# Kernel tuning notes

Measured on AMD Instinct MI355X. Metric: run time of the kernel, lower is better.

## Reference

```python
import jax, jax.numpy as jnp
import numpy as np
from jax import lax

B, S, H = 2, 1024, 1024
I = 512            # moe_intermediate_size
E = 32             # n_routed_experts
TOP_K = 4
N_GROUP = 4
TOPK_GROUP = 2
SCALE = 2.5        # routed_scaling_factor
N_SHARED = 2
SH_I = I * N_SHARED


def setup_inputs() -> dict:
    key = jax.random.key(0)
    ks = jax.random.split(key, 10)
    std = 0.02
    return {
        "hidden_states": jax.random.normal(ks[0], (B, S, H), jnp.float32),
        "router_weight": jax.random.normal(ks[1], (E, H), jnp.float32) * std,
        "router_bias": jnp.zeros((E,), jnp.float32),
        "gate_w": jax.random.normal(ks[2], (E, I, H), jnp.float32) * std,
        "up_w": jax.random.normal(ks[3], (E, I, H), jnp.float32) * std,
        "down_w": jax.random.normal(ks[4], (E, H, I), jnp.float32) * std,
        "shared_gate_w": jax.random.normal(ks[5], (SH_I, H), jnp.float32) * std,
        "shared_up_w": jax.random.normal(ks[6], (SH_I, H), jnp.float32) * std,
        "shared_down_w": jax.random.normal(ks[7], (H, SH_I), jnp.float32) * std,
    }


def _route(tokens, router_weight, router_bias):
    # tokens: [T, H] -> topk_idx [T, K] int, topk_weight [T, K] f32
    logits = tokens.astype(jnp.float32) @ router_weight.astype(jnp.float32).T  # [T, E]
    scores = jax.nn.sigmoid(logits)
    sfc = scores + router_bias[None, :]
    T = tokens.shape[0]
    # group scores: sum of top-2 per group
    grp = sfc.reshape(T, N_GROUP, E // N_GROUP)
    group_scores = lax.top_k(grp, 2)[0].sum(-1)                 # [T, n_group]
    _, gidx = lax.top_k(group_scores, TOPK_GROUP)               # [T, topk_group]
    gmask = jax.nn.one_hot(gidx, N_GROUP, dtype=sfc.dtype).sum(1)  # [T, n_group]
    smask = jnp.broadcast_to(gmask[:, :, None], (T, N_GROUP, E // N_GROUP)).reshape(T, E)
    tmp = jnp.where(smask > 0, sfc, 0.0)
    _, topk_idx = lax.top_k(tmp, TOP_K)                         # [T, K]
    topk_w = jnp.take_along_axis(scores, topk_idx, axis=1)
    topk_w = topk_w / (topk_w.sum(-1, keepdims=True) + 1e-20)   # norm_topk_prob
    topk_w = topk_w * SCALE
    return topk_idx, topk_w


def reference(hidden_states, router_weight, router_bias, gate_w, up_w, down_w,
              shared_gate_w, shared_up_w, shared_down_w):
    tokens = hidden_states.reshape(-1, H)                       # [T, H]
    topk_idx, topk_w = _route(tokens, router_weight, router_bias)
    # dense all-expert SwiGLU
    gate_vals = jax.nn.silu(jnp.einsum('th,eih->tei', tokens, gate_w))
    up_vals = jnp.einsum('th,eih->tei', tokens, up_w)
    hidden_vals = gate_vals * up_vals                           # [T, E, I]
    expert_out = jnp.einsum('tei,ehi->teh', hidden_vals, down_w)  # [T, E, H]
    sel = jnp.take_along_axis(expert_out, topk_idx[:, :, None], axis=1)  # [T, K, H]
    mixed = (sel * topk_w[:, :, None].astype(sel.dtype)).sum(1)
    mixed = mixed.reshape(hidden_states.shape)
    # shared experts (dense SwiGLU MLP)
    sg = jax.nn.silu(jnp.einsum('bsh,ih->bsi', hidden_states, shared_gate_w))
    su = jnp.einsum('bsh,ih->bsi', hidden_states, shared_up_w)
    shared = jnp.einsum('bsi,hi->bsh', sg * su, shared_down_w)
    return mixed + shared
```

## Files before the change

kernel.cpp:

```cpp
#include <hip/hip_runtime.h>
#include <hip/hip_bf16.h>
#include <math.h>

#define HD 1024
#define ID 512
#define NE 32
#define NT 2048
#define NG 4
#define SHI 1024
#define SCALE 2.5f

#define BN 64
#define BK 32
#define LDA 40

typedef __bf16 bf16_t;
typedef __attribute__((ext_vector_type(8))) __bf16 bf16x8;
typedef __attribute__((ext_vector_type(4))) __bf16 bf16x4;
typedef __attribute__((ext_vector_type(4))) float f32x4;

#define LTOK 8
#define LKC 64
__global__ void __launch_bounds__(256) logits_kernel(
    const float* __restrict__ hs, const float* __restrict__ rw,
    float* __restrict__ logits, int* __restrict__ counts)
{
    if (blockIdx.x == 0 && threadIdx.x < NE) counts[threadIdx.x] = 0;

    __shared__ float Xs[LTOK][68];
    __shared__ float Ws[NE][65];

    int tid = threadIdx.x;
    int t0 = blockIdx.x * LTOK;
    int tslot = tid >> 5, ecol = tid & 31;
    float acc = 0.f;

    for (int k0 = 0; k0 < HD; k0 += LKC) {
        if (tid < 128) {
            int row = tid >> 4, q = tid & 15;
            float4 v = *(const float4*)(hs + (size_t)(t0 + row) * HD + k0 + q * 4);
            *(float4*)(&Xs[row][q * 4]) = v;
        }
        #pragma unroll
        for (int i = 0; i < 8; ++i) {
            int idx = i * 256 + tid;
            int e = idx >> 6, kk = idx & 63;
            Ws[e][kk] = rw[(size_t)e * HD + k0 + kk];
        }
        __syncthreads();
        #pragma unroll 8
        for (int kk = 0; kk < LKC; ++kk)
            acc += Xs[tslot][kk] * Ws[ecol][kk];
        __syncthreads();
    }
    logits[(size_t)(t0 + tslot) * NE + ecol] = acc;
}

__global__ void __launch_bounds__(256) topk_kernel(
    const float* __restrict__ logits, const float* __restrict__ rb,
    float* __restrict__ topkw, int* __restrict__ counts, int* __restrict__ lists)
{
    int t = blockIdx.x * 256 + threadIdx.x;
    if (t >= NT) return;

    float scores[NE], sfc[NE], tmp[NE];
    #pragma unroll
    for (int e = 0; e < NE; ++e) {
        float l = logits[(size_t)t * NE + e];
        float s = 1.f / (1.f + __expf(-l));
        scores[e] = s;
        sfc[e] = s + rb[e];
    }
    float gs[NG];
    #pragma unroll
    for (int g = 0; g < NG; ++g) {
        float m1 = -1e30f, m2 = -1e30f;
        #pragma unroll
        for (int j = 0; j < 8; ++j) {
            float v = sfc[g * 8 + j];
            if (v > m1) { m2 = m1; m1 = v; } else if (v > m2) m2 = v;
        }
        gs[g] = m1 + m2;
    }
    int g1 = 0;
    #pragma unroll
    for (int g = 1; g < NG; ++g) if (gs[g] > gs[g1]) g1 = g;
    int g2 = -1;
    #pragma unroll
    for (int g = 0; g < NG; ++g) {
        if (g == g1) continue;
        if (g2 < 0 || gs[g] > gs[g2]) g2 = g;
    }
    #pragma unroll
    for (int e = 0; e < NE; ++e) {
        int g = e >> 3;
        tmp[e] = (g == g1 || g == g2) ? sfc[e] : 0.0f;
    }
    int idx[4]; float wk[4]; float wsum = 0.f;
    #pragma unroll
    for (int k = 0; k < 4; ++k) {
        int best = 0; float bv = -1e30f;
        #pragma unroll
        for (int e = 0; e < NE; ++e) if (tmp[e] > bv) { bv = tmp[e]; best = e; }
        idx[k] = best; tmp[best] = -1e30f;
        wk[k] = scores[best]; wsum += wk[k];
    }
    float inv = SCALE / (wsum + 1e-20f);
    #pragma unroll
    for (int k = 0; k < 4; ++k) {
        int p = t * 4 + k;
        topkw[p] = wk[k] * inv;
        int e = idx[k];
        int pos = atomicAdd(&counts[e], 1);
        lists[e * NT + pos] = p;
    }
}

__device__ inline bf16x4 cvt4(float4 v) {
    bf16x4 r;
    r[0] = (__bf16)v.x; r[1] = (__bf16)v.y; r[2] = (__bf16)v.z; r[3] = (__bf16)v.w;
    return r;
}

template<bool EXPERT, int ND, int BMT>
__global__ void __launch_bounds__(256) gateup_mfma(
    const float* __restrict__ X, const float* __restrict__ Wg,
    const float* __restrict__ Wu, bf16_t* __restrict__ Hout,
    const int* __restrict__ lists, const int* __restrict__ counts)
{
    int e = 0, cnt = NT;
    const float* wg = Wg; const float* wu = Wu;
    if (EXPERT) {
        e = blockIdx.x; cnt = counts[e];
        wg = Wg + (size_t)e * ND * HD;
        wu = Wu + (size_t)e * ND * HD;
    }
    int mtb = blockIdx.y, ntb = blockIdx.z;
    if (mtb * BMT >= cnt) return;

    __shared__ __align__(16) bf16_t As[BMT * LDA];
    __shared__ __align__(16) bf16_t Bgs[BN * LDA];
    __shared__ __align__(16) bf16_t Bus[BN * LDA];
    __shared__ int rowid[BMT];

    int tid = threadIdx.x;
    if (tid < BMT) {
        int gm = mtb * BMT + tid;
        int mm = gm < cnt ? gm : cnt - 1;
        rowid[tid] = EXPERT ? lists[e * NT + mm] : mm;
    }
    __syncthreads();

    constexpr int AR = (BMT * BK) / (256 * 4);
    constexpr int BR = (BN * BK) / (256 * 4);
    constexpr int MT = BMT / 32;

    int lane = tid & 63;
    int w = tid >> 6;
    int wm = w & 1, wn = w >> 1;
    int lrow = lane & 15, quad = lane >> 4;

    f32x4 accg[MT][2], accu[MT][2];
    #pragma unroll
    for (int i = 0; i < MT; ++i)
        #pragma unroll
        for (int j = 0; j < 2; ++j) { accg[i][j] = (f32x4){0,0,0,0}; accu[i][j] = (f32x4){0,0,0,0}; }

    float4 pa[AR], pbg[BR], pbu[BR];

    #pragma unroll
    for (int r = 0; r < AR; ++r) {
        int idx = r * 256 + tid;
        int row = idx >> 3, kq = idx & 7;
        int tok = EXPERT ? (rowid[row] >> 2) : rowid[row];
        pa[r] = *(const float4*)(X + (size_t)tok * HD + kq * 4);
    }
    #pragma unroll
    for (int r = 0; r < BR; ++r) {
        int idx = r * 256 + tid;
        int n = idx >> 3, kq = idx & 7;
        size_t off = (size_t)(ntb * BN + n) * HD + kq * 4;
        pbg[r] = *(const float4*)(wg + off);
        pbu[r] = *(const float4*)(wu + off);
    }

    for (int k0 = 0; k0 < HD; k0 += BK) {
        #pragma unroll
        for (int r = 0; r < AR; ++r) {
            int idx = r * 256 + tid;
            int row = idx >> 3, kq = idx & 7;
            *(bf16x4*)(As + row * LDA + kq * 4) = cvt4(pa[r]);
        }
        #pragma unroll
        for (int r = 0; r < BR; ++r) {
            int idx = r * 256 + tid;
            int n = idx >> 3, kq = idx & 7;
            *(bf16x4*)(Bgs + n * LDA + kq * 4) = cvt4(pbg[r]);
            *(bf16x4*)(Bus + n * LDA + kq * 4) = cvt4(pbu[r]);
        }
        __syncthreads();

        int k1 = k0 + BK;
        if (k1 < HD) {
            #pragma unroll
            for (int r = 0; r < AR; ++r) {
                int idx = r * 256 + tid;
                int row = idx >> 3, kq = idx & 7;
                int tok = EXPERT ? (rowid[row] >> 2) : rowid[row];
                pa[r] = *(const float4*)(X + (size_t)tok * HD + k1 + kq * 4);
            }
            #pragma unroll
            for (int r = 0; r < BR; ++r) {
                int idx = r * 256 + tid;
                int n = idx >> 3, kq = idx & 7;
                size_t off = (size_t)(ntb * BN + n) * HD + k1 + kq * 4;
                pbg[r] = *(const float4*)(wg + off);
                pbu[r] = *(const float4*)(wu + off);
            }
        }

        bf16x8 af[MT], bg[2], bu[2];
        #pragma unroll
        for (int mt = 0; mt < MT; ++mt)
            af[mt] = *(const bf16x8*)(As + (wm * (BMT / 2) + mt * 16 + lrow) * LDA + quad * 8);
        #pragma unroll
        for (int nt = 0; nt < 2; ++nt) {
            bg[nt] = *(const bf16x8*)(Bgs + (wn * 32 + nt * 16 + lrow) * LDA + quad * 8);
            bu[nt] = *(const bf16x8*)(Bus + (wn * 32 + nt * 16 + lrow) * LDA + quad * 8);
        }
        #pragma unroll
        for (int mt = 0; mt < MT; ++mt)
            #pragma unroll
            for (int nt = 0; nt < 2; ++nt) {
                accg[mt][nt] = __builtin_amdgcn_mfma_f32_16x16x32_bf16(af[mt], bg[nt], accg[mt][nt], 0, 0, 0);
                accu[mt][nt] = __builtin_amdgcn_mfma_f32_16x16x32_bf16(af[mt], bu[nt], accu[mt][nt], 0, 0, 0);
            }
        __syncthreads();
    }

    #pragma unroll
    for (int mt = 0; mt < MT; ++mt)
        #pragma unroll
        for (int r = 0; r < 4; ++r) {
            int row_local = wm * (BMT / 2) + mt * 16 + quad * 4 + r;
            int gm = mtb * BMT + row_local;
            if (gm >= cnt) continue;
            int p = rowid[row_local];
            #pragma unroll
            for (int nt = 0; nt < 2; ++nt) {
                int col = ntb * BN + wn * 32 + nt * 16 + lrow;
                float g = accg[mt][nt][r], u = accu[mt][nt][r];
                float h = (g / (1.f + __expf(-g))) * u;
                Hout[(size_t)p * ND + col] = (__bf16)h;
            }
        }
}

template<bool EXPERT, int KD, int BMT>
__global__ void __launch_bounds__(256) down_mfma(
    const bf16_t* __restrict__ Hin, const float* __restrict__ Wd,
    float* __restrict__ out, const int* __restrict__ lists,
    const int* __restrict__ counts, const float* __restrict__ topkw)
{
    int e = 0, cnt = NT;
    const float* wd = Wd;
    if (EXPERT) {
        e = blockIdx.x; cnt = counts[e];
        wd = Wd + (size_t)e * HD * KD;
    }
    int mtb = blockIdx.y, ntb = blockIdx.z;
    if (mtb * BMT >= cnt) return;

    __shared__ __align__(16) bf16_t As[BMT * LDA];
    __shared__ __align__(16) bf16_t Ws[BN * LDA];
    __shared__ int rowid[BMT];

    int tid = threadIdx.x;
    if (tid < BMT) {
        int gm = mtb * BMT + tid;
        int mm = gm < cnt ? gm : cnt - 1;
        rowid[tid] = EXPERT ? lists[e * NT + mm] : mm;
    }
    __syncthreads();

    constexpr int ARH = (BMT * BK / 8) / 256;
    constexpr int BR = (BN * BK) / (256 * 4);
    constexpr int MT = BMT / 32;

    int lane = tid & 63;
    int w = tid >> 6;
    int wm = w & 1, wn = w >> 1;
    int lrow = lane & 15, quad = lane >> 4;

    f32x4 acc[MT][2];
    #pragma unroll
    for (int i = 0; i < MT; ++i)
        #pragma unroll
        for (int j = 0; j < 2; ++j) acc[i][j] = (f32x4){0,0,0,0};

    bf16x8 pa[ARH];
    float4 pw[BR];

    #pragma unroll
    for (int r = 0; r < ARH; ++r) {
        int idx = r * 256 + tid;
        int row = idx >> 2, c = idx & 3;
        pa[r] = *(const bf16x8*)(Hin + (size_t)rowid[row] * KD + c * 8);
    }
    #pragma unroll
    for (int r = 0; r < BR; ++r) {
        int idx = r * 256 + tid;
        int n = idx >> 3, kq = idx & 7;
        pw[r] = *(const float4*)(wd + (size_t)(ntb * BN + n) * KD + kq * 4);
    }

    for (int k0 = 0; k0 < KD; k0 += BK) {
        #pragma unroll
        for (int r = 0; r < ARH; ++r) {
            int idx = r * 256 + tid;
            int row = idx >> 2, c = idx & 3;
            *(bf16x8*)(As + row * LDA + c * 8) = pa[r];
        }
        #pragma unroll
        for (int r = 0; r < BR; ++r) {
            int idx = r * 256 + tid;
            int n = idx >> 3, kq = idx & 7;
            *(bf16x4*)(Ws + n * LDA + kq * 4) = cvt4(pw[r]);
        }
        __syncthreads();

        int k1 = k0 + BK;
        if (k1 < KD) {
            #pragma unroll
            for (int r = 0; r < ARH; ++r) {
                int idx = r * 256 + tid;
                int row = idx >> 2, c = idx & 3;
                pa[r] = *(const bf16x8*)(Hin + (size_t)rowid[row] * KD + k1 + c * 8);
            }
            #pragma unroll
            for (int r = 0; r < BR; ++r) {
                int idx = r * 256 + tid;
                int n = idx >> 3, kq = idx & 7;
                pw[r] = *(const float4*)(wd + (size_t)(ntb * BN + n) * KD + k1 + kq * 4);
            }
        }

        bf16x8 af[MT], bf[2];
        #pragma unroll
        for (int mt = 0; mt < MT; ++mt)
            af[mt] = *(const bf16x8*)(As + (wm * (BMT / 2) + mt * 16 + lrow) * LDA + quad * 8);
        #pragma unroll
        for (int nt = 0; nt < 2; ++nt)
            bf[nt] = *(const bf16x8*)(Ws + (wn * 32 + nt * 16 + lrow) * LDA + quad * 8);
        #pragma unroll
        for (int mt = 0; mt < MT; ++mt)
            #pragma unroll
            for (int nt = 0; nt < 2; ++nt)
                acc[mt][nt] = __builtin_amdgcn_mfma_f32_16x16x32_bf16(af[mt], bf[nt], acc[mt][nt], 0, 0, 0);
        __syncthreads();
    }

    #pragma unroll
    for (int mt = 0; mt < MT; ++mt)
        #pragma unroll
        for (int r = 0; r < 4; ++r) {
            int row_local = wm * (BMT / 2) + mt * 16 + quad * 4 + r;
            int gm = mtb * BMT + row_local;
            if (gm >= cnt) continue;
            int p = rowid[row_local];
            #pragma unroll
            for (int nt = 0; nt < 2; ++nt) {
                int col = ntb * BN + wn * 32 + nt * 16 + lrow;
                float val = acc[mt][nt][r];
                if (EXPERT) {
                    float wgt = topkw[p];
                    atomicAdd(&out[(size_t)(p >> 2) * HD + col], wgt * val);
                } else {
                    out[(size_t)p * HD + col] = val;
                }
            }
        }
}

extern "C" void kernel_launch(void* const* d_in, const int* in_sizes, int n_in,
                              void* d_out, int out_size, void* d_ws, size_t ws_size,
                              hipStream_t stream) {
    const float* hs  = (const float*)d_in[0];
    const float* rw  = (const float*)d_in[1];
    const float* rb  = (const float*)d_in[2];
    const float* gw  = (const float*)d_in[3];
    const float* uw  = (const float*)d_in[4];
    const float* dw  = (const float*)d_in[5];
    const float* sgw = (const float*)d_in[6];
    const float* suw = (const float*)d_in[7];
    const float* sdw = (const float*)d_in[8];
    float* out = (float*)d_out;

    char* ws = (char*)d_ws;
    int*    counts = (int*)ws;
    float*  topkw  = (float*)(ws + 128);
    int*    lists  = (int*)(ws + 128 + 32768);
    float*  logits = (float*)(ws + 128 + 32768 + 262144);
    bf16_t* hbuf   = (bf16_t*)(ws + 128 + 32768 + 262144 + 262144);

    logits_kernel<<<NT / LTOK, 256, 0, stream>>>(hs, rw, logits, counts);
    topk_kernel<<<NT / 256, 256, 0, stream>>>(logits, rb, topkw, counts, lists);

    gateup_mfma<false, SHI, 64><<<dim3(1, NT / 64, SHI / BN), 256, 0, stream>>>(
        hs, sgw, suw, hbuf, nullptr, nullptr);
    down_mfma<false, SHI, 64><<<dim3(1, NT / 64, HD / BN), 256, 0, stream>>>(
        hbuf, sdw, out, nullptr, nullptr, nullptr);

    gateup_mfma<true, ID, 128><<<dim3(NE, NT / 128, ID / BN), 256, 0, stream>>>(
        hs, gw, uw, hbuf, lists, counts);
    down_mfma<true, ID, 128><<<dim3(NE, NT / 128, HD / BN), 256, 0, stream>>>(
        hbuf, dw, out, lists, counts, topkw);
}
```

Measured before the change: 418.5 us.

## Preconvert weights to bf16 and use LDS-direct double-buffered MFMA GEMMs

Adds a pass that converts all expert, shared weights and activations to bf16 in workspace. New gate-up and down GEMM kernels then load tiles with global_load_lds into swizzled, double-buffered shared memory. The goal is to remove per-tile fp32 conversion and register staging from the GEMM inner loops and to overlap loads with MFMA. In exchange, each call does an extra full read/write pass over the weights and needs a large workspace, falling back to the old path otherwise.

```diff
diff --git a/kernel.cpp b/kernel.cpp
--- a/kernel.cpp
+++ b/kernel.cpp
@@ -19,6 +19,42 @@
 typedef __attribute__((ext_vector_type(4))) __bf16 bf16x4;
 typedef __attribute__((ext_vector_type(4))) float f32x4;
 
+__device__ __forceinline__ void gld16(const bf16_t* g, bf16_t* l) {
+    __builtin_amdgcn_global_load_lds(
+        (__attribute__((address_space(1))) void*)g,
+        (__attribute__((address_space(3))) void*)l,
+        16, 0, 0);
+}
+
+#define CH_G 2097152LL
+#define CH_S 131072LL
+#define CH_H 262144LL
+#define CH_TOT (3*CH_G + 3*CH_S + CH_H)
+
+__global__ void __launch_bounds__(256) convert_all(
+    const float* __restrict__ g, const float* __restrict__ u, const float* __restrict__ d,
+    const float* __restrict__ sg, const float* __restrict__ su, const float* __restrict__ sd,
+    const float* __restrict__ hs, bf16_t* __restrict__ dst)
+{
+    for (long long c = blockIdx.x * 256LL + threadIdx.x; c < CH_TOT; c += (long long)gridDim.x * 256LL) {
+        const float* src;
+        long long r = c;
+        if (r < CH_G)                   src = g  + (size_t)r * 8;
+        else if ((r -= CH_G) < CH_G)    src = u  + (size_t)r * 8;
+        else if ((r -= CH_G) < CH_G)    src = d  + (size_t)r * 8;
+        else if ((r -= CH_G) < CH_S)    src = sg + (size_t)r * 8;
+        else if ((r -= CH_S) < CH_S)    src = su + (size_t)r * 8;
+        else if ((r -= CH_S) < CH_S)    src = sd + (size_t)r * 8;
+        else { r -= CH_S;               src = hs + (size_t)r * 8; }
+        float4 a = *(const float4*)src;
+        float4 b = *(const float4*)(src + 4);
+        bf16x8 o;
+        o[0] = (__bf16)a.x; o[1] = (__bf16)a.y; o[2] = (__bf16)a.z; o[3] = (__bf16)a.w;
+        o[4] = (__bf16)b.x; o[5] = (__bf16)b.y; o[6] = (__bf16)b.z; o[7] = (__bf16)b.w;
+        *(bf16x8*)(dst + (size_t)c * 8) = o;
+    }
+}
+
 #define LTOK 8
 #define LKC 64
 __global__ void __launch_bounds__(256) logits_kernel(
@@ -115,6 +151,257 @@
         lists[e * NT + pos] = p;
     }
 }
+
+
+template<bool EXPERT, int ND, int BMT>
+__global__ void __launch_bounds__(256) gateup2(
+    const bf16_t* __restrict__ X, const bf16_t* __restrict__ Wg,
+    const bf16_t* __restrict__ Wu, bf16_t* __restrict__ Hout,
+    const int* __restrict__ lists, const int* __restrict__ counts)
+{
+    constexpr int NB = 64;
+    int e = 0, cnt = NT;
+    const bf16_t* wg = Wg; const bf16_t* wu = Wu;
+    if (EXPERT) {
+        e = blockIdx.x; cnt = counts[e];
+        wg = Wg + (size_t)e * ND * HD;
+        wu = Wu + (size_t)e * ND * HD;
+    }
+    int mtb = blockIdx.y, ntb = blockIdx.z;
+    if (mtb * BMT >= cnt) return;
+
+    constexpr int AU = BMT / 64;
+    constexpr int MT = BMT / 32;
+
+    __shared__ __align__(16) bf16_t As[2][BMT * BK];
+    __shared__ __align__(16) bf16_t Bgs[2][NB * BK];
+    __shared__ __align__(16) bf16_t Bus[2][NB * BK];
+    __shared__ int rowid[BMT];
+
+    int tid = threadIdx.x;
+    if (tid < BMT) {
+        int gm = mtb * BMT + tid;
+        int mm = gm < cnt ? gm : cnt - 1;
+        rowid[tid] = EXPERT ? lists[e * NT + mm] : mm;
+    }
+    __syncthreads();
+
+    int lane = tid & 63;
+    int w = tid >> 6;
+    int wm = w & 1, wn = w >> 1;
+    int lrow = lane & 15, quad = lane >> 4;
+    int chunkL = lane & 3;
+
+    const bf16_t* asrc[AU];
+    #pragma unroll
+    for (int i = 0; i < AU; ++i) {
+        int row = (w * AU + i) * 16 + (lane >> 2);
+        int tok = EXPERT ? (rowid[row] >> 2) : rowid[row];
+        int ch = chunkL ^ ((row >> 1) & 3);
+        asrc[i] = X + (size_t)tok * HD + ch * 8;
+    }
+    int nrow = w * 16 + (lane >> 2);
+    int nch = chunkL ^ ((nrow >> 1) & 3);
+    const bf16_t* bgsrc = wg + (size_t)(ntb * NB + nrow) * HD + nch * 8;
+    const bf16_t* busrc = wu + (size_t)(ntb * NB + nrow) * HD + nch * 8;
+
+    int aoff[MT], goff[2];
+    #pragma unroll
+    for (int mt = 0; mt < MT; ++mt) {
+        int row = wm * (BMT / 2) + mt * 16 + lrow;
+        aoff[mt] = row * BK + (quad ^ ((row >> 1) & 3)) * 8;
+    }
+    #pragma unroll
+    for (int nt = 0; nt < 2; ++nt) {
+        int row = wn * 32 + nt * 16 + lrow;
+        goff[nt] = row * BK + (quad ^ ((row >> 1) & 3)) * 8;
+    }
+
+    f32x4 accg[MT][2], accu[MT][2];
+    #pragma unroll
+    for (int i = 0; i < MT; ++i)
+        #pragma unroll
+        for (int j = 0; j < 2; ++j) { accg[i][j] = (f32x4){0,0,0,0}; accu[i][j] = (f32x4){0,0,0,0}; }
+
+    auto stage = [&](int buf, int k) {
+        #pragma unroll
+        for (int i = 0; i < AU; ++i)
+            gld16(asrc[i] + k, &As[buf][(w * AU + i) * 512]);
+        gld16(bgsrc + k, &Bgs[buf][w * 512]);
+        gld16(busrc + k, &Bus[buf][w * 512]);
+    };
+    auto compute = [&](int buf) {
+        bf16x8 af[MT], bg[2], bu[2];
+        #pragma unroll
+        for (int mt = 0; mt < MT; ++mt) af[mt] = *(const bf16x8*)(&As[buf][aoff[mt]]);
+        #pragma unroll
+        for (int nt = 0; nt < 2; ++nt) {
+            bg[nt] = *(const bf16x8*)(&Bgs[buf][goff[nt]]);
+            bu[nt] = *(const bf16x8*)(&Bus[buf][goff[nt]]);
+        }
+        #pragma unroll
+        for (int mt = 0; mt < MT; ++mt)
+            #pragma unroll
+            for (int nt = 0; nt < 2; ++nt) {
+                accg[mt][nt] = __builtin_amdgcn_mfma_f32_16x16x32_bf16(af[mt], bg[nt], accg[mt][nt], 0, 0, 0);
+                accu[mt][nt] = __builtin_amdgcn_mfma_f32_16x16x32_bf16(af[mt], bu[nt], accu[mt][nt], 0, 0, 0);
+            }
+    };
+
+    stage(0, 0);
+    __syncthreads();
+    int buf = 0;
+    for (int k0 = BK; k0 < HD; k0 += BK) {
+        stage(buf ^ 1, k0);
+        compute(buf);
+        __syncthreads();
+        buf ^= 1;
+    }
+    compute(buf);
+
+    #pragma unroll
+    for (int mt = 0; mt < MT; ++mt)
+        #pragma unroll
+        for (int r = 0; r < 4; ++r) {
+            int row_local = wm * (BMT / 2) + mt * 16 + quad * 4 + r;
+            int gm = mtb * BMT + row_local;
+            if (gm >= cnt) continue;
+            int p = rowid[row_local];
+            #pragma unroll
+            for (int nt = 0; nt < 2; ++nt) {
+                int col = ntb * NB + wn * 32 + nt * 16 + lrow;
+                float g = accg[mt][nt][r], u = accu[mt][nt][r];
+                float h = (g / (1.f + __expf(-g))) * u;
+                Hout[(size_t)p * ND + col] = (__bf16)h;
+            }
+        }
+}
+
+template<bool EXPERT, int KD, int BMT, int NB>
+__global__ void __launch_bounds__(256) down2(
+    const bf16_t* __restrict__ Hin, const bf16_t* __restrict__ Wd,
+    float* __restrict__ out, const int* __restrict__ lists,
+    const int* __restrict__ counts, const float* __restrict__ topkw)
+{
+    int e = 0, cnt = NT;
+    const bf16_t* wd = Wd;
+    if (EXPERT) {
+        e = blockIdx.x; cnt = counts[e];
+        wd = Wd + (size_t)e * HD * KD;
+    }
+    int mtb = blockIdx.y, ntb = blockIdx.z;
+    if (mtb * BMT >= cnt) return;
+
+    constexpr int AU = BMT / 64;
+    constexpr int BU = NB / 64;
+    constexpr int MT = BMT / 32;
+    constexpr int NTF = NB / 32;
+
+    __shared__ __align__(16) bf16_t As[2][BMT * BK];
+    __shared__ __align__(16) bf16_t Ws[2][NB * BK];
+    __shared__ int rowid[BMT];
+
+    int tid = threadIdx.x;
+    if (tid < BMT) {
+        int gm = mtb * BMT + tid;
+        int mm = gm < cnt ? gm : cnt - 1;
+        rowid[tid] = EXPERT ? lists[e * NT + mm] : mm;
+    }
+    __syncthreads();
+
+    int lane = tid & 63;
+    int w = tid >> 6;
+    int wm = w & 1, wn = w >> 1;
+    int lrow = lane & 15, quad = lane >> 4;
+    int chunkL = lane & 3;
+
+    const bf16_t* asrc[AU];
+    #pragma unroll
+    for (int i = 0; i < AU; ++i) {
+        int row = (w * AU + i) * 16 + (lane >> 2);
+        int ch = chunkL ^ ((row >> 1) & 3);
+        asrc[i] = Hin + (size_t)rowid[row] * KD + ch * 8;
+    }
+    const bf16_t* wsrc[BU];
+    #pragma unroll
+    for (int i = 0; i < BU; ++i) {
+        int row = (w * BU + i) * 16 + (lane >> 2);
+        int ch = chunkL ^ ((row >> 1) & 3);
+        wsrc[i] = wd + (size_t)(ntb * NB + row) * KD + ch * 8;
+    }
+
+    int aoff[MT], woff[NTF];
+    #pragma unroll
+    for (int mt = 0; mt < MT; ++mt) {
+        int row = wm * (BMT / 2) + mt * 16 + lrow;
+        aoff[mt] = row * BK + (quad ^ ((row >> 1) & 3)) * 8;
+    }
+    #pragma unroll
+    for (int nt = 0; nt < NTF; ++nt) {
+        int row = wn * (NB / 2) + nt * 16 + lrow;
+        woff[nt] = row * BK + (quad ^ ((row >> 1) & 3)) * 8;
+    }
+
+    f32x4 acc[MT][NTF];
+    #pragma unroll
+    for (int i = 0; i < MT; ++i)
+        #pragma unroll
+        for (int j = 0; j < NTF; ++j) acc[i][j] = (f32x4){0,0,0,0};
+
+    auto stage = [&](int buf, int k) {
+        #pragma unroll
+        for (int i = 0; i < AU; ++i)
+            gld16(asrc[i] + k, &As[buf][(w * AU + i) * 512]);
+        #pragma unroll
+        for (int i = 0; i < BU; ++i)
+            gld16(wsrc[i] + k, &Ws[buf][(w * BU + i) * 512]);
+    };
+    auto compute = [&](int buf) {
+        bf16x8 af[MT], br[NTF];
+        #pragma unroll
+        for (int mt = 0; mt < MT; ++mt) af[mt] = *(const bf16x8*)(&As[buf][aoff[mt]]);
+        #pragma unroll
+        for (int nt = 0; nt < NTF; ++nt) br[nt] = *(const bf16x8*)(&Ws[buf][woff[nt]]);
+        #pragma unroll
+        for (int mt = 0; mt < MT; ++mt)
+            #pragma unroll
+            for (int nt = 0; nt < NTF; ++nt)
+                acc[mt][nt] = __builtin_amdgcn_mfma_f32_16x16x32_bf16(af[mt], br[nt], acc[mt][nt], 0, 0, 0);
+    };
+
+    stage(0, 0);
+    __syncthreads();
+    int buf = 0;
+    for (int k0 = BK; k0 < KD; k0 += BK) {
+        stage(buf ^ 1, k0);
+        compute(buf);
+        __syncthreads();
+        buf ^= 1;
+    }
+    compute(buf);
+
+    #pragma unroll
+    for (int mt = 0; mt < MT; ++mt)
+        #pragma unroll
+        for (int r = 0; r < 4; ++r) {
+            int row_local = wm * (BMT / 2) + mt * 16 + quad * 4 + r;
+            int gm = mtb * BMT + row_local;
+            if (gm >= cnt) continue;
+            int p = rowid[row_local];
+            #pragma unroll
+            for (int nt = 0; nt < NTF; ++nt) {
+                int col = ntb * NB + wn * (NB / 2) + nt * 16 + lrow;
+                float val = acc[mt][nt][r];
+                if (EXPERT) {
+                    float wgt = topkw[p];
+                    atomicAdd(&out[(size_t)(p >> 2) * HD + col], wgt * val);
+                } else {
+                    out[(size_t)p * HD + col] = val;
+                }
+            }
+        }
+}
+
 
 __device__ inline bf16x4 cvt4(float4 v) {
     bf16x4 r;
@@ -345,18 +632,18 @@
             }
         }
 
-        bf16x8 af[MT], bf[2];
+        bf16x8 af[MT], bfr[2];
         #pragma unroll
         for (int mt = 0; mt < MT; ++mt)
             af[mt] = *(const bf16x8*)(As + (wm * (BMT / 2) + mt * 16 + lrow) * LDA + quad * 8);
         #pragma unroll
         for (int nt = 0; nt < 2; ++nt)
-            bf[nt] = *(const bf16x8*)(Ws + (wn * 32 + nt * 16 + lrow) * LDA + quad * 8);
+            bfr[nt] = *(const bf16x8*)(Ws + (wn * 32 + nt * 16 + lrow) * LDA + quad * 8);
         #pragma unroll
         for (int mt = 0; mt < MT; ++mt)
             #pragma unroll
             for (int nt = 0; nt < 2; ++nt)
-                acc[mt][nt] = __builtin_amdgcn_mfma_f32_16x16x32_bf16(af[mt], bf[nt], acc[mt][nt], 0, 0, 0);
+                acc[mt][nt] = __builtin_amdgcn_mfma_f32_16x16x32_bf16(af[mt], bfr[nt], acc[mt][nt], 0, 0, 0);
         __syncthreads();
     }
 
@@ -395,24 +682,60 @@
     const float* suw = (const float*)d_in[7];
     const float* sdw = (const float*)d_in[8];
     float* out = (float*)d_out;
-
     char* ws = (char*)d_ws;
-    int*    counts = (int*)ws;
-    float*  topkw  = (float*)(ws + 128);
-    int*    lists  = (int*)(ws + 128 + 32768);
-    float*  logits = (float*)(ws + 128 + 32768 + 262144);
-    bf16_t* hbuf   = (bf16_t*)(ws + 128 + 32768 + 262144 + 262144);
-
-    logits_kernel<<<NT / LTOK, 256, 0, stream>>>(hs, rw, logits, counts);
-    topk_kernel<<<NT / 256, 256, 0, stream>>>(logits, rb, topkw, counts, lists);
-
-    gateup_mfma<false, SHI, 64><<<dim3(1, NT / 64, SHI / BN), 256, 0, stream>>>(
-        hs, sgw, suw, hbuf, nullptr, nullptr);
-    down_mfma<false, SHI, 64><<<dim3(1, NT / 64, HD / BN), 256, 0, stream>>>(
-        hbuf, sdw, out, nullptr, nullptr, nullptr);
-
-    gateup_mfma<true, ID, 128><<<dim3(NE, NT / 128, ID / BN), 256, 0, stream>>>(
-        hs, gw, uw, hbuf, lists, counts);
-    down_mfma<true, ID, 128><<<dim3(NE, NT / 128, HD / BN), 256, 0, stream>>>(
-        hbuf, dw, out, lists, counts, topkw);
-}
+
+    constexpr size_t BF16_ELEMS = (size_t)3 * NE * ID * HD
+                                + (size_t)3 * SHI * HD
+                                + (size_t)NT * HD;
+    constexpr size_t REQ_WS = (size_t)(1 << 20) + BF16_ELEMS * 2 + (size_t)8192 * ID * 2;
+
+    if (ws_size >= REQ_WS) {
+        int*    counts = (int*)ws;
+        float*  topkw  = (float*)(ws + 1024);
+        int*    lists  = (int*)(ws + 1024 + 32768);
+        float*  logits = (float*)(ws + 1024 + 32768 + 262144);
+
+        bf16_t* wg_b = (bf16_t*)(ws + (1 << 20));
+        bf16_t* wu_b = wg_b + (size_t)NE * ID * HD;
+        bf16_t* wd_b = wu_b + (size_t)NE * ID * HD;
+        bf16_t* sg_b = wd_b + (size_t)NE * ID * HD;
+        bf16_t* su_b = sg_b + (size_t)SHI * HD;
+        bf16_t* sd_b = su_b + (size_t)SHI * HD;
+        bf16_t* hs_b = sd_b + (size_t)SHI * HD;
+        bf16_t* hbuf = hs_b + (size_t)NT * HD;
+
+        convert_all<<<2048, 256, 0, stream>>>(gw, uw, dw, sgw, suw, sdw, hs, wg_b);
+
+        logits_kernel<<<NT / LTOK, 256, 0, stream>>>(hs, rw, logits, counts);
+        topk_kernel<<<NT / 256, 256, 0, stream>>>(logits, rb, topkw, counts, lists);
+
+        gateup2<false, SHI, 64><<<dim3(1, NT / 64, SHI / 64), 256, 0, stream>>>(
+            hs_b, sg_b, su_b, hbuf, nullptr, nullptr);
+        down2<false, SHI, 64, 64><<<dim3(1, NT / 64, HD / 64), 256, 0, stream>>>(
+            hbuf, sd_b, out, nullptr, nullptr, nullptr);
+
+        gateup2<true, ID, 128><<<dim3(NE, NT / 128, ID / 64), 256, 0, stream>>>(
+            hs_b, wg_b, wu_b, hbuf, lists, counts);
+        down2<true, ID, 128, 128><<<dim3(NE, NT / 128, HD / 128), 256, 0, stream>>>(
+            hbuf, wd_b, out, lists, counts, topkw);
+    } else {
+        int*    counts = (int*)ws;
+        float*  topkw  = (float*)(ws + 128);
+        int*    lists  = (int*)(ws + 128 + 32768);
+        float*  logits = (float*)(ws + 128 + 32768 + 262144);
+        bf16_t* hbuf   = (bf16_t*)(ws + 128 + 32768 + 262144 + 262144);
+
+        logits_kernel<<<NT / LTOK, 256, 0, stream>>>(hs, rw, logits, counts);
+        topk_kernel<<<NT / 256, 256, 0, stream>>>(logits, rb, topkw, counts, lists);
+
+        gateup_mfma<false, SHI, 64><<<dim3(1, NT / 64, SHI / BN), 256, 0, stream>>>(
+            hs, sgw, suw, hbuf, nullptr, nullptr);
+        down_mfma<false, SHI, 64><<<dim3(1, NT / 64, HD / BN), 256, 0, stream>>>(
+            hbuf, sdw, out, nullptr, nullptr, nullptr);
+
+        gateup_mfma<true, ID, 128><<<dim3(NE, NT / 128, ID / BN), 256, 0, stream>>>(
+            hs, gw, uw, hbuf, lists, counts);
+        down_mfma<true, ID, 128><<<dim3(NE, NT / 128, HD / BN), 256, 0, stream>>>(
+            hbuf, dw, out, lists, counts, topkw);
+    }
+}
```

Result: faster. 406.9 us (-2.8%).

## Merge shared and routed experts into persistent weight-stationary gate-up and down kernels

Applied to the files above, without the earlier changes.

Adds new gateup_f32 and down_f32 kernels. Each block owns a fixed 32-column weight slice, for an expert or for the shared MLP, and loops over all of that expert's token tiles. The slice stays cache-resident across M tiles, and shared and routed work are merged into one launch per stage. The output is now zeroed inside the logits kernel so both down paths can accumulate atomically. This relies on a larger workspace and falls back to the old path if it is too small. The risk is load imbalance, since per-block work scales with expert token count, and the shared-expert blocks do full-size loops.

```diff
diff --git a/kernel.cpp b/kernel.cpp
--- a/kernel.cpp
+++ b/kernel.cpp
@@ -10,27 +10,42 @@
 #define SHI 1024
 #define SCALE 2.5f
 
-#define BN 64
 #define BK 32
 #define LDA 40
+#define BN 64
 
 typedef __bf16 bf16_t;
 typedef __attribute__((ext_vector_type(8))) __bf16 bf16x8;
 typedef __attribute__((ext_vector_type(4))) __bf16 bf16x4;
 typedef __attribute__((ext_vector_type(4))) float f32x4;
 
+__device__ inline bf16x4 cvt4(float4 v) {
+    bf16x4 r;
+    r[0] = (__bf16)v.x; r[1] = (__bf16)v.y; r[2] = (__bf16)v.z; r[3] = (__bf16)v.w;
+    return r;
+}
+
 #define LTOK 8
 #define LKC 64
 __global__ void __launch_bounds__(256) logits_kernel(
     const float* __restrict__ hs, const float* __restrict__ rw,
-    float* __restrict__ logits, int* __restrict__ counts)
+    float* __restrict__ logits, int* __restrict__ counts,
+    float* __restrict__ outz)
 {
-    if (blockIdx.x == 0 && threadIdx.x < NE) counts[threadIdx.x] = 0;
+    int tid = threadIdx.x;
+    if (blockIdx.x == 0 && tid < NE) counts[tid] = 0;
+
+    {
+        size_t base = ((size_t)blockIdx.x * 256 + tid) * 32;
+        float4 z = {0.f, 0.f, 0.f, 0.f};
+        float4* p = (float4*)(outz + base);
+        #pragma unroll
+        for (int i = 0; i < 8; ++i) p[i] = z;
+    }
 
     __shared__ float Xs[LTOK][68];
     __shared__ float Ws[NE][65];
 
-    int tid = threadIdx.x;
     int t0 = blockIdx.x * LTOK;
     int tslot = tid >> 5, ecol = tid & 31;
     float acc = 0.f;
@@ -116,11 +131,241 @@
     }
 }
 
-__device__ inline bf16x4 cvt4(float4 v) {
-    bf16x4 r;
-    r[0] = (__bf16)v.x; r[1] = (__bf16)v.y; r[2] = (__bf16)v.z; r[3] = (__bf16)v.w;
-    return r;
-}
+
+__global__ void __launch_bounds__(256, 3) gateup_f32(
+    const float* __restrict__ hs,
+    const float* __restrict__ gw, const float* __restrict__ uw,
+    const float* __restrict__ sgw, const float* __restrict__ suw,
+    bf16_t* __restrict__ hr, bf16_t* __restrict__ hsh,
+    const int* __restrict__ lists, const int* __restrict__ counts)
+{
+    constexpr int BM = 128, NS = HD / BK;
+    int bx = blockIdx.x, tid = threadIdx.x;
+
+    int cnt, nb0, ND;
+    const float *wg, *wu;
+    bf16_t* hout;
+    const int* rlist = nullptr;
+    if (bx < 512) {
+        int e = bx >> 4; cnt = counts[e];
+        nb0 = (bx & 15) * 32;
+        wg = gw + (size_t)e * ID * HD;
+        wu = uw + (size_t)e * ID * HD;
+        hout = hr; ND = ID;
+        rlist = lists + e * NT;
+    } else {
+        cnt = NT; nb0 = (bx - 512) * 32;
+        wg = sgw; wu = suw;
+        hout = hsh; ND = SHI;
+    }
+
+    __shared__ __align__(16) bf16_t As[2][BM * LDA];
+    __shared__ __align__(16) bf16_t Bgs[2][32 * LDA];
+    __shared__ __align__(16) bf16_t Bus[2][32 * LDA];
+    __shared__ int rowid[BM];
+
+    int lane = tid & 63, w = tid >> 6;
+    int lrow = lane & 15, quad = lane >> 4;
+    int tr = tid >> 3, tc = tid & 7;
+
+    const float* bgb = wg + (size_t)(nb0 + tr) * HD + tc * 4;
+    const float* bub = wu + (size_t)(nb0 + tr) * HD + tc * 4;
+
+    for (int m0 = 0; m0 < cnt; m0 += BM) {
+        __syncthreads();
+        if (tid < BM) {
+            int gm = m0 + tid;
+            int mm = gm < cnt ? gm : cnt - 1;
+            rowid[tid] = rlist ? rlist[mm] : mm;
+        }
+        __syncthreads();
+
+        const float* ab[4];
+        #pragma unroll
+        for (int rr = 0; rr < 4; ++rr) {
+            int row = rr * 32 + tr;
+            int tok = rlist ? (rowid[row] >> 2) : rowid[row];
+            ab[rr] = hs + (size_t)tok * HD + tc * 4;
+        }
+
+        f32x4 accg[2][2], accu[2][2];
+        #pragma unroll
+        for (int i = 0; i < 2; ++i)
+            #pragma unroll
+            for (int j = 0; j < 2; ++j) { accg[i][j] = (f32x4){0,0,0,0}; accu[i][j] = (f32x4){0,0,0,0}; }
+
+        float4 a[4], bgq, buq;
+        #pragma unroll
+        for (int rr = 0; rr < 4; ++rr) a[rr] = *(const float4*)(ab[rr]);
+        bgq = *(const float4*)(bgb);
+        buq = *(const float4*)(bub);
+
+        for (int ks = 0; ks < NS; ++ks) {
+            int buf = ks & 1;
+            #pragma unroll
+            for (int rr = 0; rr < 4; ++rr)
+                *(bf16x4*)(&As[buf][(rr * 32 + tr) * LDA + tc * 4]) = cvt4(a[rr]);
+            *(bf16x4*)(&Bgs[buf][tr * LDA + tc * 4]) = cvt4(bgq);
+            *(bf16x4*)(&Bus[buf][tr * LDA + tc * 4]) = cvt4(buq);
+            __syncthreads();
+            if (ks + 1 < NS) {
+                int k = (ks + 1) * BK;
+                #pragma unroll
+                for (int rr = 0; rr < 4; ++rr) a[rr] = *(const float4*)(ab[rr] + k);
+                bgq = *(const float4*)(bgb + k);
+                buq = *(const float4*)(bub + k);
+            }
+            bf16x8 af[2], bgf[2], buf_[2];
+            #pragma unroll
+            for (int mt = 0; mt < 2; ++mt)
+                af[mt] = *(const bf16x8*)(&As[buf][(w * 32 + mt * 16 + lrow) * LDA + quad * 8]);
+            #pragma unroll
+            for (int nt = 0; nt < 2; ++nt) {
+                bgf[nt]  = *(const bf16x8*)(&Bgs[buf][(nt * 16 + lrow) * LDA + quad * 8]);
+                buf_[nt] = *(const bf16x8*)(&Bus[buf][(nt * 16 + lrow) * LDA + quad * 8]);
+            }
+            #pragma unroll
+            for (int mt = 0; mt < 2; ++mt)
+                #pragma unroll
+                for (int nt = 0; nt < 2; ++nt) {
+                    accg[mt][nt] = __builtin_amdgcn_mfma_f32_16x16x32_bf16(af[mt], bgf[nt],  accg[mt][nt], 0, 0, 0);
+                    accu[mt][nt] = __builtin_amdgcn_mfma_f32_16x16x32_bf16(af[mt], buf_[nt], accu[mt][nt], 0, 0, 0);
+                }
+        }
+
+        #pragma unroll
+        for (int mt = 0; mt < 2; ++mt)
+            #pragma unroll
+            for (int r = 0; r < 4; ++r) {
+                int row_local = w * 32 + mt * 16 + quad * 4 + r;
+                int gm = m0 + row_local;
+                if (gm >= cnt) continue;
+                int p = rowid[row_local];
+                #pragma unroll
+                for (int nt = 0; nt < 2; ++nt) {
+                    int col = nb0 + nt * 16 + lrow;
+                    float gv = accg[mt][nt][r], uv = accu[mt][nt][r];
+                    float h = (gv / (1.f + __expf(-gv))) * uv;
+                    hout[(size_t)p * ND + col] = (__bf16)h;
+                }
+            }
+    }
+}
+
+__global__ void __launch_bounds__(256, 3) down_f32(
+    const bf16_t* __restrict__ hr, const bf16_t* __restrict__ hsh,
+    const float* __restrict__ dwf, const float* __restrict__ sdwf,
+    float* __restrict__ out,
+    const int* __restrict__ lists, const int* __restrict__ counts,
+    const float* __restrict__ topkw)
+{
+    constexpr int BM = 128;
+    int bx = blockIdx.x, tid = threadIdx.x;
+
+    int cnt, nb0, KD;
+    const bf16_t* Hin;
+    const float* wd;
+    const int* rlist = nullptr;
+    bool routed;
+    if (bx < 1024) {
+        int e = bx >> 5; cnt = counts[e];
+        nb0 = (bx & 31) * 32;
+        Hin = hr; wd = dwf + (size_t)e * HD * ID; KD = ID;
+        rlist = lists + e * NT; routed = true;
+    } else {
+        cnt = NT; nb0 = (bx - 1024) * 32;
+        Hin = hsh; wd = sdwf; KD = SHI; routed = false;
+    }
+    int NS = KD / BK;
+
+    __shared__ __align__(16) bf16_t As[2][BM * LDA];
+    __shared__ __align__(16) bf16_t Ws[2][32 * LDA];
+    __shared__ int rowid[BM];
+
+    int lane = tid & 63, w = tid >> 6;
+    int lrow = lane & 15, quad = lane >> 4;
+    int tr = tid >> 3, tc = tid & 7;
+
+    const float* wb = wd + (size_t)(nb0 + tr) * KD + tc * 4;
+
+    for (int m0 = 0; m0 < cnt; m0 += BM) {
+        __syncthreads();
+        if (tid < BM) {
+            int gm = m0 + tid;
+            int mm = gm < cnt ? gm : cnt - 1;
+            rowid[tid] = rlist ? rlist[mm] : mm;
+        }
+        __syncthreads();
+
+        const bf16_t* ab[2];
+        int arow_[2], ach_[2];
+        #pragma unroll
+        for (int rr = 0; rr < 2; ++rr) {
+            int idx = rr * 256 + tid;
+            arow_[rr] = idx >> 2; ach_[rr] = idx & 3;
+            ab[rr] = Hin + (size_t)rowid[arow_[rr]] * KD + ach_[rr] * 8;
+        }
+
+        f32x4 acc[2][2];
+        #pragma unroll
+        for (int i = 0; i < 2; ++i)
+            #pragma unroll
+            for (int j = 0; j < 2; ++j) acc[i][j] = (f32x4){0,0,0,0};
+
+        bf16x8 a2[2]; float4 wq;
+        #pragma unroll
+        for (int rr = 0; rr < 2; ++rr) a2[rr] = *(const bf16x8*)(ab[rr]);
+        wq = *(const float4*)(wb);
+
+        for (int ks = 0; ks < NS; ++ks) {
+            int buf = ks & 1;
+            #pragma unroll
+            for (int rr = 0; rr < 2; ++rr)
+                *(bf16x8*)(&As[buf][arow_[rr] * LDA + ach_[rr] * 8]) = a2[rr];
+            *(bf16x4*)(&Ws[buf][tr * LDA + tc * 4]) = cvt4(wq);
+            __syncthreads();
+            if (ks + 1 < NS) {
+                int k = (ks + 1) * BK;
+                #pragma unroll
+                for (int rr = 0; rr < 2; ++rr) a2[rr] = *(const bf16x8*)(ab[rr] + k);
+                wq = *(const float4*)(wb + k);
+            }
+            bf16x8 af[2], wf[2];
+            #pragma unroll
+            for (int mt = 0; mt < 2; ++mt)
+                af[mt] = *(const bf16x8*)(&As[buf][(w * 32 + mt * 16 + lrow) * LDA + quad * 8]);
+            #pragma unroll
+            for (int nt = 0; nt < 2; ++nt)
+                wf[nt] = *(const bf16x8*)(&Ws[buf][(nt * 16 + lrow) * LDA + quad * 8]);
+            #pragma unroll
+            for (int mt = 0; mt < 2; ++mt)
+                #pragma unroll
+                for (int nt = 0; nt < 2; ++nt)
+                    acc[mt][nt] = __builtin_amdgcn_mfma_f32_16x16x32_bf16(af[mt], wf[nt], acc[mt][nt], 0, 0, 0);
+        }
+
+        #pragma unroll
+        for (int mt = 0; mt < 2; ++mt)
+            #pragma unroll
+            for (int r = 0; r < 4; ++r) {
+                int row_local = w * 32 + mt * 16 + quad * 4 + r;
+                int gm = m0 + row_local;
+                if (gm >= cnt) continue;
+                int p = rowid[row_local];
+                #pragma unroll
+                for (int nt = 0; nt < 2; ++nt) {
+                    int col = nb0 + nt * 16 + lrow;
+                    float val = acc[mt][nt][r];
+                    if (routed) {
+                        atomicAdd(&out[(size_t)(p >> 2) * HD + col], topkw[p] * val);
+                    } else {
+                        atomicAdd(&out[(size_t)p * HD + col], val);
+                    }
+                }
+            }
+    }
+}
+
 
 template<bool EXPERT, int ND, int BMT>
 __global__ void __launch_bounds__(256) gateup_mfma(
@@ -345,18 +590,18 @@
             }
         }
 
-        bf16x8 af[MT], bf[2];
+        bf16x8 af[MT], bfr[2];
         #pragma unroll
         for (int mt = 0; mt < MT; ++mt)
             af[mt] = *(const bf16x8*)(As + (wm * (BMT / 2) + mt * 16 + lrow) * LDA + quad * 8);
         #pragma unroll
         for (int nt = 0; nt < 2; ++nt)
-            bf[nt] = *(const bf16x8*)(Ws + (wn * 32 + nt * 16 + lrow) * LDA + quad * 8);
+            bfr[nt] = *(const bf16x8*)(Ws + (wn * 32 + nt * 16 + lrow) * LDA + quad * 8);
         #pragma unroll
         for (int mt = 0; mt < MT; ++mt)
             #pragma unroll
             for (int nt = 0; nt < 2; ++nt)
-                acc[mt][nt] = __builtin_amdgcn_mfma_f32_16x16x32_bf16(af[mt], bf[nt], acc[mt][nt], 0, 0, 0);
+                acc[mt][nt] = __builtin_amdgcn_mfma_f32_16x16x32_bf16(af[mt], bfr[nt], acc[mt][nt], 0, 0, 0);
         __syncthreads();
     }
 
@@ -395,24 +640,42 @@
     const float* suw = (const float*)d_in[7];
     const float* sdw = (const float*)d_in[8];
     float* out = (float*)d_out;
-
     char* ws = (char*)d_ws;
-    int*    counts = (int*)ws;
-    float*  topkw  = (float*)(ws + 128);
-    int*    lists  = (int*)(ws + 128 + 32768);
-    float*  logits = (float*)(ws + 128 + 32768 + 262144);
-    bf16_t* hbuf   = (bf16_t*)(ws + 128 + 32768 + 262144 + 262144);
-
-    logits_kernel<<<NT / LTOK, 256, 0, stream>>>(hs, rw, logits, counts);
-    topk_kernel<<<NT / 256, 256, 0, stream>>>(logits, rb, topkw, counts, lists);
-
-    gateup_mfma<false, SHI, 64><<<dim3(1, NT / 64, SHI / BN), 256, 0, stream>>>(
-        hs, sgw, suw, hbuf, nullptr, nullptr);
-    down_mfma<false, SHI, 64><<<dim3(1, NT / 64, HD / BN), 256, 0, stream>>>(
-        hbuf, sdw, out, nullptr, nullptr, nullptr);
-
-    gateup_mfma<true, ID, 128><<<dim3(NE, NT / 128, ID / BN), 256, 0, stream>>>(
-        hs, gw, uw, hbuf, lists, counts);
-    down_mfma<true, ID, 128><<<dim3(NE, NT / 128, HD / BN), 256, 0, stream>>>(
-        hbuf, dw, out, lists, counts, topkw);
-}
+
+    constexpr size_t HR_B  = (size_t)NT * 4 * ID * 2;
+    constexpr size_t HSH_B = (size_t)NT * SHI * 2;
+    constexpr size_t REQ_WS = (size_t)(1 << 20) + HR_B + HSH_B;
+
+    if (ws_size >= REQ_WS) {
+        int*    counts = (int*)ws;
+        float*  topkw  = (float*)(ws + 1024);
+        int*    lists  = (int*)(ws + 1024 + 32768);
+        float*  logits = (float*)(ws + 1024 + 32768 + 262144);
+        bf16_t* hr     = (bf16_t*)(ws + (1 << 20));
+        bf16_t* hsh    = (bf16_t*)(ws + (1 << 20) + HR_B);
+
+        logits_kernel<<<NT / LTOK, 256, 0, stream>>>(hs, rw, logits, counts, out);
+        topk_kernel<<<NT / 256, 256, 0, stream>>>(logits, rb, topkw, counts, lists);
+        gateup_f32<<<544, 256, 0, stream>>>(hs, gw, uw, sgw, suw, hr, hsh, lists, counts);
+        down_f32<<<1056, 256, 0, stream>>>(hr, hsh, dw, sdw, out, lists, counts, topkw);
+    } else {
+        int*    counts = (int*)ws;
+        float*  topkw  = (float*)(ws + 128);
+        int*    lists  = (int*)(ws + 128 + 32768);
+        float*  logits = (float*)(ws + 128 + 32768 + 262144);
+        bf16_t* hbuf   = (bf16_t*)(ws + 128 + 32768 + 262144 + 262144);
+
+        logits_kernel<<<NT / LTOK, 256, 0, stream>>>(hs, rw, logits, counts, out);
+        topk_kernel<<<NT / 256, 256, 0, stream>>>(logits, rb, topkw, counts, lists);
+
+        gateup_mfma<false, SHI, 64><<<dim3(1, NT / 64, SHI / BN), 256, 0, stream>>>(
+            hs, sgw, suw, hbuf, nullptr, nullptr);
+        down_mfma<false, SHI, 64><<<dim3(1, NT / 64, HD / BN), 256, 0, stream>>>(
+            hbuf, sdw, out, nullptr, nullptr, nullptr);
+
+        gateup_mfma<true, ID, 128><<<dim3(NE, NT / 128, ID / BN), 256, 0, stream>>>(
+            hs, gw, uw, hbuf, lists, counts);
+        down_mfma<true, ID, 128><<<dim3(NE, NT / 128, HD / BN), 256, 0, stream>>>(
+            hbuf, dw, out, lists, counts, topkw);
+    }
+}
```

Measured after the change: 958.9 us. +129.2%, slower.
